# Optimization experiments

Hardware: AMD Instinct MI355X
Metric: run time of the kernel (lower is better)

Reference implementation:

```python
import jax, jax.numpy as jnp
import numpy as np

B, L_IN, D_MODEL, CONV_D, KSIZE = 16, 512, 384, 1536, 3
MEL_MAX = 4096
LN_EPS = 1e-5


def _conv1d_same(h, w, b):
    # h: [B, C_in, L], w: [C_out, C_in, K] -> [B, C_out, L]
    y = jax.lax.conv_general_dilated(h, w, window_strides=(1,), padding='SAME',
                                     dimension_numbers=('NCH', 'OIH', 'NCH'))
    return y + b[None, :, None]


def _layernorm(x, g, b):
    m = jnp.mean(x, -1, keepdims=True)
    v = jnp.mean((x - m) ** 2, -1, keepdims=True)
    return (x - m) * jax.lax.rsqrt(v + LN_EPS) * g + b


def _ffn(x, wa, ba, wb, bb):
    # Conv1D_FFT: conv(d_model->conv_d) ReLU conv(conv_d->d_model) ReLU
    h = jnp.transpose(x, (0, 2, 1))
    h = jax.nn.relu(_conv1d_same(h, wa, ba))
    h = jax.nn.relu(_conv1d_same(h, wb, bb))
    return jnp.transpose(h, (0, 2, 1))


def _dur_pred(x, w1, b1, w2, b2, g1, be1, w3, b3, w4, b4, g2, be2, wl, bl):
    h = _ffn(x, w1, b1, w2, b2)
    h = _layernorm(h, g1, be1)  # dropout is identity at eval
    h = _ffn(h, w3, b3, w4, b4)
    h = _layernorm(h, g2, be2)
    return (h @ wl + bl)[..., 0]  # [B, L_in], squeeze(-1)


def _length_regulate(x, dur, mel_max_len):
    # Equivalent to alignment @ x where alignment[b,t,j]=1 iff cum[b,j-1] <= t < cum[b,j],
    # padded with zeros out to mel_max_len (original pads output to mel_max_len).
    cum = jnp.cumsum(dur, axis=-1)                        # [B, L_in]
    total = cum[:, -1]                                    # [B]
    t = jnp.arange(mel_max_len, dtype=cum.dtype)          # [T]
    idx = jax.vmap(lambda c: jnp.searchsorted(c, t, side='right'))(cum)  # [B, T]
    idx = jnp.minimum(idx, x.shape[1] - 1)
    out = jnp.take_along_axis(x, idx[:, :, None], axis=1)  # [B, T, D]
    mask = (t[None, :] < total[:, None])[..., None]
    return out * mask


def setup_inputs() -> dict:
    key = jax.random.key(0)
    ks = jax.random.split(key, 8)
    def nrm(k, shape):
        return jax.random.normal(k, shape, jnp.float32) * 0.02
    return {
        'x': jax.random.normal(ks[0], (B, L_IN, D_MODEL), jnp.float32),
        'target': jax.random.randint(ks[1], (B, L_IN), 0, 8, jnp.int32),
        'mel_max_len': MEL_MAX,
        'w1': nrm(ks[2], (CONV_D, D_MODEL, KSIZE)), 'b1': jnp.zeros((CONV_D,), jnp.float32),
        'w2': nrm(ks[3], (D_MODEL, CONV_D, KSIZE)), 'b2': jnp.zeros((D_MODEL,), jnp.float32),
        'g1': jnp.ones((D_MODEL,), jnp.float32), 'be1': jnp.zeros((D_MODEL,), jnp.float32),
        'w3': nrm(ks[4], (CONV_D, D_MODEL, KSIZE)), 'b3': jnp.zeros((CONV_D,), jnp.float32),
        'w4': nrm(ks[5], (D_MODEL, CONV_D, KSIZE)), 'b4': jnp.zeros((D_MODEL,), jnp.float32),
        'g2': jnp.ones((D_MODEL,), jnp.float32), 'be2': jnp.zeros((D_MODEL,), jnp.float32),
        'wl': nrm(ks[6], (D_MODEL, 1)), 'bl': jnp.zeros((1,), jnp.float32),
    }


def reference(x, target, mel_max_len, w1, b1, w2, b2, g1, be1, w3, b3, w4, b4, g2, be2, wl, bl):
    dur_preds = _dur_pred(x, w1, b1, w2, b2, g1, be1, w3, b3, w4, b4, g2, be2, wl, bl)
    output = _length_regulate(x, target, mel_max_len)
    return (output, dur_preds)
```

## Files before the change

### kernel.cpp

```cpp
#include <hip/hip_runtime.h>
#include <hip/hip_bf16.h>
#include <cstddef>
#include <cstdint>

#define NB 16
#define LIN 512
#define DM 384
#define DC 1536
#define MELMAX 4096
#define LN_EPS 1e-5f

typedef __bf16 bf16x8 __attribute__((ext_vector_type(8)));
typedef float f32x4 __attribute__((ext_vector_type(4)));

#define GL2LDS(gp, lp)                                                                \
    __builtin_amdgcn_global_load_lds((const __attribute__((address_space(1))) void*)(gp), \
                                     (__attribute__((address_space(3))) void*)(lp), 16, 0, 0)

__device__ __forceinline__ float wred(float v) {
#pragma unroll
    for (int m = 32; m >= 1; m >>= 1) v += __shfl_xor(v, m, 64);
    return v;
}

__device__ __forceinline__ unsigned short f2bf(float f) {
    __hip_bfloat16 h = __float2bfloat16(f);
    return *reinterpret_cast<unsigned short*>(&h);
}

__device__ __forceinline__ float bf2f(unsigned short u) {
    return __uint_as_float(((unsigned)u) << 16);
}


__global__ void cumsum_kernel(const int* __restrict__ tgt, int* __restrict__ cum) {
    __shared__ int s[LIN];
    const int b = blockIdx.x, tid = threadIdx.x;
    s[tid] = tgt[b * LIN + tid];
    __syncthreads();
    for (int off = 1; off < LIN; off <<= 1) {
        int v = (tid >= off) ? s[tid - off] : 0;
        __syncthreads();
        s[tid] += v;
        __syncthreads();
    }
    cum[b * LIN + tid] = s[tid];
}


__global__ __launch_bounds__(256) void gather_kernel(const float* __restrict__ x,
                                                     const int* __restrict__ cum,
                                                     float* __restrict__ out) {
    const int wid = (blockIdx.x * 256 + threadIdx.x) >> 6;
    const int lane = threadIdx.x & 63;
    const int b = wid >> 12;
    const int t = wid & (MELMAX - 1);
    const int* c = cum + b * LIN;
    const int total = c[LIN - 1];
    float4* orow = reinterpret_cast<float4*>(out + ((size_t)b * MELMAX + t) * DM);
    if (t < total) {
        int lo = 0, hi = LIN;
        while (lo < hi) { int mid = (lo + hi) >> 1; if (c[mid] > t) hi = mid; else lo = mid + 1; }
        const int idx = lo < (LIN - 1) ? lo : (LIN - 1);
        const float4* xrow = reinterpret_cast<const float4*>(x + ((size_t)b * LIN + idx) * DM);
#pragma unroll
        for (int j = 0; j < 2; ++j) {
            const int p = lane + 64 * j;
            if (p < DM / 4) orow[p] = xrow[p];
        }
    } else {
        const float4 z = make_float4(0.f, 0.f, 0.f, 0.f);
#pragma unroll
        for (int j = 0; j < 2; ++j) {
            const int p = lane + 64 * j;
            if (p < DM / 4) orow[p] = z;
        }
    }
}


#define ZPAD_BLKS 96
#define CASTX_BLKS 3072
#define WCAST_BLKS 2304

__global__ void prep_kernel(const float* __restrict__ x, unsigned short* __restrict__ xb,
                            unsigned short* __restrict__ hbig, unsigned short* __restrict__ h2b,
                            const float* __restrict__ w1, const float* __restrict__ w2,
                            const float* __restrict__ w3, const float* __restrict__ w4,
                            unsigned short* __restrict__ o1, unsigned short* __restrict__ o2,
                            unsigned short* __restrict__ o3, unsigned short* __restrict__ o4) {
    const int bid = blockIdx.x, tid = threadIdx.x;
    if (bid < ZPAD_BLKS) {
        const int buf = bid >> 5, rem = bid & 31;
        const int b = rem >> 1, row = (rem & 1) ? (LIN + 1) : 0;
        unsigned short* p = buf == 0 ? xb : (buf == 1 ? hbig : h2b);
        const int rl = buf == 1 ? DC : DM;
        unsigned short* base = p + ((size_t)b * (LIN + 2) + row) * rl;
        for (int c = tid; c < rl; c += 256) base[c] = 0;
        return;
    }
    if (bid < ZPAD_BLKS + CASTX_BLKS) {
        const int idx = (bid - ZPAD_BLKS) * 256 + tid;
        const float4 v = reinterpret_cast<const float4*>(x)[idx];
        const int e = idx * 4;
        const int b = e / (LIN * DM);
        const int rem = e - b * (LIN * DM);
        const int l = rem / DM;
        const int c = rem - l * DM;
        ushort4 o;
        o.x = f2bf(v.x); o.y = f2bf(v.y); o.z = f2bf(v.z); o.w = f2bf(v.w);
        *reinterpret_cast<ushort4*>(xb + ((size_t)b * (LIN + 2) + l + 1) * DM + c) = o;
        return;
    }
    const int j = bid - ZPAD_BLKS - CASTX_BLKS;
    const int which = j / WCAST_BLKS;
    const int idx = (j - which * WCAST_BLKS) * 256 + tid;
    const float* w = which == 0 ? w1 : which == 1 ? w2 : which == 2 ? w3 : w4;
    unsigned short* gg = which == 0 ? o1 : which == 1 ? o2 : which == 2 ? o3 : o4;
    const int CI = (which == 0 || which == 2) ? DM : DC;
    const int co = idx / CI, ci = idx - co * CI;
    const float* p = w + (size_t)idx * 3;
    unsigned short* o = gg + (size_t)co * (3 * CI) + ci;
    o[0 * CI] = f2bf(p[0]);
    o[1 * CI] = f2bf(p[1]);
    o[2 * CI] = f2bf(p[2]);
}


template <int CI, int CO, int BN>
__global__ __launch_bounds__(256, 2) void conv_mfma_kernel(const unsigned short* __restrict__ in,
                                                           const unsigned short* __restrict__ wg,
                                                           const float* __restrict__ bias,
                                                           unsigned short* __restrict__ out) {
    constexpr int BM = 128, BK = 32;
    constexpr int KC = CI / BK;
    constexpr int AGRP = 12;
    constexpr int GPT = BN / 16;
    constexpr int BGRP = 3 * GPT;
    constexpr int NW_N = BN / 32;
    constexpr int NT = CO / BN;
    constexpr int NCONV = NB * (LIN / BM) * NT;

    __shared__ __align__(16) unsigned short As[2][AGRP * 512];
    __shared__ __align__(16) unsigned short Bs[2][BGRP * 512];

    const int tid = threadIdx.x;
    const int lane = tid & 63;
    const int wv = tid >> 6;

    const int orig = blockIdx.x;
    const int q = NCONV >> 3, xcd = orig & 7, o = orig >> 3;
    const int wgid = xcd * q + o;

    const int mg = wgid / NT;
    const int nt = wgid - mg * NT;
    const int b = mg >> 2;
    const int l0 = (mg & 3) * BM;
    const int n0 = nt * BN;

    const int wr = wv >> 1, wc = wv & 1;

    const unsigned short* inb = in + (size_t)b * (LIN + 2) * CI;

    f32x4 acc[4][NW_N];
#pragma unroll
    for (int m = 0; m < 4; ++m)
#pragma unroll
        for (int n = 0; n < NW_N; ++n) acc[m][n] = (f32x4){0.f, 0.f, 0.f, 0.f};

    const int lrow = lane >> 2;
    const int lch = lane & 3;
    const int fr = lane & 15, kg = lane >> 4;

    const unsigned short* aroot = inb + (size_t)l0 * CI + lch * 8;
    const unsigned short* broot = wg + (size_t)n0 * (3 * CI) + lch * 8;

#define STAGE(c, kb)                                                                      \
    do {                                                                                  \
        const unsigned short* abase = aroot + (kb) * BK;                                  \
        _Pragma("unroll")                                                                 \
        for (int g = wv; g < AGRP; g += 4) {                                              \
            const int sg = g < 9 ? g : 0;    \
            GL2LDS(abase + (size_t)(sg * 16 + lrow) * CI, &As[c][g * 512]);               \
        }                                                                                 \
        const unsigned short* bbase = broot + (kb) * BK;                                  \
        _Pragma("unroll")                                                                 \
        for (int g2 = wv; g2 < BGRP; g2 += 4) {                                           \
            const int t = g2 / GPT, gr = g2 - t * GPT;                                    \
            GL2LDS(bbase + (size_t)(gr * 16 + lrow) * (3 * CI) + (size_t)t * CI,          \
                   &Bs[c][g2 * 512]);                                                     \
        }                                                                                 \
    } while (0)

#define COMPUTE(c)                                                                        \
    do {                                                                                  \
        _Pragma("unroll")                                                                 \
        for (int t = 0; t < 3; ++t) {                                                     \
            bf16x8 aF[4], bF[NW_N];                                                       \
            _Pragma("unroll")                                                             \
            for (int m = 0; m < 4; ++m)                                                   \
                aF[m] = *reinterpret_cast<const bf16x8*>(                                 \
                    &As[c][(t + wr * 64 + m * 16 + fr) * BK + kg * 8]);                   \
            _Pragma("unroll")                                                             \
            for (int n = 0; n < NW_N; ++n)                                                \
                bF[n] = *reinterpret_cast<const bf16x8*>(                                 \
                    &Bs[c][(t * BN + wc * (BN / 2) + n * 16 + fr) * BK + kg * 8]);        \
            _Pragma("unroll")                                                             \
            for (int m = 0; m < 4; ++m)                                                   \
                _Pragma("unroll")                                                         \
                for (int n = 0; n < NW_N; ++n)                                            \
                    acc[m][n] =                                                           \
                        __builtin_amdgcn_mfma_f32_16x16x32_bf16(aF[m], bF[n], acc[m][n],  \
                                                                0, 0, 0);                 \
        }                                                                                 \
    } while (0)

    STAGE(0, 0);
    STAGE(1, 1);
#pragma unroll 1
    for (int kb = 0; kb < KC; ++kb) {
        const int cur = kb & 1;
        if constexpr (BN == 128)
            asm volatile("s_waitcnt vmcnt(9)" ::: "memory");
        else
            asm volatile("s_waitcnt vmcnt(6)" ::: "memory");
        __builtin_amdgcn_sched_barrier(0);
        __builtin_amdgcn_s_barrier();
        __builtin_amdgcn_sched_barrier(0);
        COMPUTE(cur);
        asm volatile("s_waitcnt lgkmcnt(0)" ::: "memory");
        __builtin_amdgcn_sched_barrier(0);
        __builtin_amdgcn_s_barrier();
        __builtin_amdgcn_sched_barrier(0);
        int nk = kb + 2;
        if (nk >= KC) nk -= KC;
        STAGE(cur, nk);
    }
#undef STAGE
#undef COMPUTE

    const int fq = lane >> 4;
    float bv[NW_N];
#pragma unroll
    for (int n = 0; n < NW_N; ++n) bv[n] = bias[n0 + wc * (BN / 2) + n * 16 + fr];
    unsigned short* outb = out + (size_t)b * (LIN + 2) * CO;
#pragma unroll
    for (int m = 0; m < 4; ++m)
#pragma unroll
        for (int qy = 0; qy < 4; ++qy) {
            const int grow = l0 + wr * 64 + m * 16 + fq * 4 + qy + 1;
            unsigned short* orow = outb + (size_t)grow * CO + n0 + wc * (BN / 2) + fr;
#pragma unroll
            for (int n = 0; n < NW_N; ++n) {
                const float v = fmaxf(acc[m][n][qy] + bv[n], 0.f);
                orow[n * 16] = f2bf(v);
            }
        }
}


__global__ void ln_kernel(unsigned short* __restrict__ h, const float* __restrict__ g,
                          const float* __restrict__ be) {
    const int row = blockIdx.x, lane = threadIdx.x;
    const int b = row >> 9, l = row & (LIN - 1);
    unsigned short* hr = h + ((size_t)b * (LIN + 2) + l + 1) * DM;
    float v[6];
    float s = 0.f;
#pragma unroll
    for (int j = 0; j < 6; ++j) { v[j] = bf2f(hr[lane + 64 * j]); s += v[j]; }
    s = wred(s);
    const float mean = s * (1.f / DM);
    float vs = 0.f;
#pragma unroll
    for (int j = 0; j < 6; ++j) { const float d = v[j] - mean; vs += d * d; }
    vs = wred(vs);
    const float rstd = rsqrtf(vs * (1.f / DM) + LN_EPS);
#pragma unroll
    for (int j = 0; j < 6; ++j) {
        const int c = lane + 64 * j;
        hr[c] = f2bf((v[j] - mean) * rstd * g[c] + be[c]);
    }
}


__global__ void ln_linear_kernel(const unsigned short* __restrict__ h, const float* __restrict__ g,
                                 const float* __restrict__ be, const float* __restrict__ wl,
                                 const float* __restrict__ bl, float* __restrict__ dur) {
    const int row = blockIdx.x, lane = threadIdx.x;
    const int b = row >> 9, l = row & (LIN - 1);
    const unsigned short* hr = h + ((size_t)b * (LIN + 2) + l + 1) * DM;
    float v[6];
    float s = 0.f;
#pragma unroll
    for (int j = 0; j < 6; ++j) { v[j] = bf2f(hr[lane + 64 * j]); s += v[j]; }
    s = wred(s);
    const float mean = s * (1.f / DM);
    float vs = 0.f;
#pragma unroll
    for (int j = 0; j < 6; ++j) { const float d = v[j] - mean; vs += d * d; }
    vs = wred(vs);
    const float rstd = rsqrtf(vs * (1.f / DM) + LN_EPS);
    float dot = 0.f;
#pragma unroll
    for (int j = 0; j < 6; ++j) {
        const int c = lane + 64 * j;
        dot += ((v[j] - mean) * rstd * g[c] + be[c]) * wl[c];
    }
    dot = wred(dot);
    if (lane == 0) dur[row] = dot + bl[0];
}


extern "C" void kernel_launch(void* const* d_in, const int* in_sizes, int n_in,
                              void* d_out, int out_size, void* d_ws, size_t ws_size,
                              hipStream_t stream) {
    const float* x   = (const float*)d_in[0];
    const int*   tgt = (const int*)d_in[1];
    const float* w1  = (const float*)d_in[3];
    const float* b1  = (const float*)d_in[4];
    const float* w2  = (const float*)d_in[5];
    const float* b2  = (const float*)d_in[6];
    const float* g1  = (const float*)d_in[7];
    const float* be1 = (const float*)d_in[8];
    const float* w3  = (const float*)d_in[9];
    const float* b3  = (const float*)d_in[10];
    const float* w4  = (const float*)d_in[11];
    const float* b4  = (const float*)d_in[12];
    const float* g2  = (const float*)d_in[13];
    const float* be2 = (const float*)d_in[14];
    const float* wl  = (const float*)d_in[15];
    const float* bl  = (const float*)d_in[16];

    float* out = (float*)d_out;
    float* dur = out + (size_t)NB * MELMAX * DM;

    unsigned short* ws = (unsigned short*)d_ws;
    unsigned short* xb   = ws;
    unsigned short* hbig = xb + (size_t)NB * (LIN + 2) * DM;
    unsigned short* h2b  = hbig + (size_t)NB * (LIN + 2) * DC;
    unsigned short* wg1  = h2b + (size_t)NB * (LIN + 2) * DM;
    unsigned short* wg2  = wg1 + (size_t)DC * 3 * DM;
    unsigned short* wg3  = wg2 + (size_t)DM * 3 * DC;
    unsigned short* wg4  = wg3 + (size_t)DC * 3 * DM;
    int* cum = (int*)(wg4 + (size_t)DM * 3 * DC);

    cumsum_kernel<<<NB, LIN, 0, stream>>>(tgt, cum);
    gather_kernel<<<(NB * MELMAX) / 4, 256, 0, stream>>>(x, cum, out);

    prep_kernel<<<ZPAD_BLKS + CASTX_BLKS + 4 * WCAST_BLKS, 256, 0, stream>>>(
        x, xb, hbig, h2b, w1, w2, w3, w4, wg1, wg2, wg3, wg4);

    conv_mfma_kernel<DM, DC, 128><<<NB * (LIN / 128) * (DC / 128), 256, 0, stream>>>(xb, wg1, b1, hbig);
    conv_mfma_kernel<DC, DM, 64><<<NB * (LIN / 128) * (DM / 64), 256, 0, stream>>>(hbig, wg2, b2, h2b);
    ln_kernel<<<NB * LIN, 64, 0, stream>>>(h2b, g1, be1);
    conv_mfma_kernel<DM, DC, 128><<<NB * (LIN / 128) * (DC / 128), 256, 0, stream>>>(h2b, wg3, b3, hbig);
    conv_mfma_kernel<DC, DM, 64><<<NB * (LIN / 128) * (DM / 64), 256, 0, stream>>>(hbig, wg4, b4, xb);
    ln_linear_kernel<<<NB * LIN, 64, 0, stream>>>(xb, g2, be2, wl, bl, dur);
}
```

Baseline: 223.9 us.

## Swizzle conv LDS tiles, fix BN at 64, raise occupancy and MFMA priority

Fixes the conv tile width at 64 for all four convolutions, which doubles the block count for the d_model to conv_d convs. It trims the A-tile halo groups from 12 to 9, which removes the dummy duplicate loads. It applies an XOR swizzle to A-tile LDS columns and stores B tiles in a fragment-major layout to reduce LDS bank conflicts on the fragment reads. It also raises launch bounds to 3 blocks per CU, wraps MFMAs in s_setprio, and adjusts vmcnt waits per wave to match the new per-wave load counts. The narrower tile costs more A-tile reloads for the wide convs.

```diff
diff --git a/kernel.cpp b/kernel.cpp
--- a/kernel.cpp
+++ b/kernel.cpp
@@ -127,14 +127,14 @@
 }
 
 
-template <int CI, int CO, int BN>
-__global__ __launch_bounds__(256, 2) void conv_mfma_kernel(const unsigned short* __restrict__ in,
+template <int CI, int CO>
+__global__ __launch_bounds__(256, 3) void conv_mfma_kernel(const unsigned short* __restrict__ in,
                                                            const unsigned short* __restrict__ wg,
                                                            const float* __restrict__ bias,
                                                            unsigned short* __restrict__ out) {
-    constexpr int BM = 128, BK = 32;
+    constexpr int BM = 128, BN = 64, BK = 32;
     constexpr int KC = CI / BK;
-    constexpr int AGRP = 12;
+    constexpr int AGRP = 9;
     constexpr int GPT = BN / 16;
     constexpr int BGRP = 3 * GPT;
     constexpr int NW_N = BN / 32;
@@ -172,22 +172,23 @@
     const int lch = lane & 3;
     const int fr = lane & 15, kg = lane >> 4;
 
-    const unsigned short* aroot = inb + (size_t)l0 * CI + lch * 8;
-    const unsigned short* broot = wg + (size_t)n0 * (3 * CI) + lch * 8;
+    const unsigned short* aroot = inb + (size_t)l0 * CI;
+    const unsigned short* broot = wg + (size_t)n0 * (3 * CI);
+
+    const int aswz = (lch ^ (lrow & 3)) * 8;
+    const int bfr = lane & 15, bkg = lane >> 4;
 
 #define STAGE(c, kb)                                                                      \
     do {                                                                                  \
         const unsigned short* abase = aroot + (kb) * BK;                                  \
         _Pragma("unroll")                                                                 \
-        for (int g = wv; g < AGRP; g += 4) {                                              \
-            const int sg = g < 9 ? g : 0;    \
-            GL2LDS(abase + (size_t)(sg * 16 + lrow) * CI, &As[c][g * 512]);               \
-        }                                                                                 \
+        for (int g = wv; g < AGRP; g += 4)                                                \
+            GL2LDS(abase + (size_t)(g * 16 + lrow) * CI + aswz, &As[c][g * 512]);         \
         const unsigned short* bbase = broot + (kb) * BK;                                  \
         _Pragma("unroll")                                                                 \
         for (int g2 = wv; g2 < BGRP; g2 += 4) {                                           \
             const int t = g2 / GPT, gr = g2 - t * GPT;                                    \
-            GL2LDS(bbase + (size_t)(gr * 16 + lrow) * (3 * CI) + (size_t)t * CI,          \
+            GL2LDS(bbase + (size_t)(gr * 16 + bfr) * (3 * CI) + (size_t)t * CI + bkg * 8, \
                    &Bs[c][g2 * 512]);                                                     \
         }                                                                                 \
     } while (0)
@@ -198,13 +199,16 @@
         for (int t = 0; t < 3; ++t) {                                                     \
             bf16x8 aF[4], bF[NW_N];                                                       \
             _Pragma("unroll")                                                             \
-            for (int m = 0; m < 4; ++m)                                                   \
+            for (int m = 0; m < 4; ++m) {                                                 \
+                const int r = t + wr * 64 + m * 16 + fr;                                  \
                 aF[m] = *reinterpret_cast<const bf16x8*>(                                 \
-                    &As[c][(t + wr * 64 + m * 16 + fr) * BK + kg * 8]);                   \
+                    &As[c][r * BK + ((kg ^ (r & 3)) * 8)]);                               \
+            }                                                                             \
             _Pragma("unroll")                                                             \
             for (int n = 0; n < NW_N; ++n)                                                \
                 bF[n] = *reinterpret_cast<const bf16x8*>(                                 \
-                    &Bs[c][(t * BN + wc * (BN / 2) + n * 16 + fr) * BK + kg * 8]);        \
+                    &Bs[c][(t * GPT + wc * NW_N + n) * 512 + kg * 128 + fr * 8]);         \
+            __builtin_amdgcn_s_setprio(1);                                                \
             _Pragma("unroll")                                                             \
             for (int m = 0; m < 4; ++m)                                                   \
                 _Pragma("unroll")                                                         \
@@ -212,6 +216,7 @@
                     acc[m][n] =                                                           \
                         __builtin_amdgcn_mfma_f32_16x16x32_bf16(aF[m], bF[n], acc[m][n],  \
                                                                 0, 0, 0);                 \
+            __builtin_amdgcn_s_setprio(0);                                                \
         }                                                                                 \
     } while (0)
 
@@ -220,10 +225,10 @@
 #pragma unroll 1
     for (int kb = 0; kb < KC; ++kb) {
         const int cur = kb & 1;
-        if constexpr (BN == 128)
-            asm volatile("s_waitcnt vmcnt(9)" ::: "memory");
+        if (wv == 0)
+            asm volatile("s_waitcnt vmcnt(6)" ::: "memory");
         else
-            asm volatile("s_waitcnt vmcnt(6)" ::: "memory");
+            asm volatile("s_waitcnt vmcnt(5)" ::: "memory");
         __builtin_amdgcn_sched_barrier(0);
         __builtin_amdgcn_s_barrier();
         __builtin_amdgcn_sched_barrier(0);
@@ -350,10 +355,10 @@
     prep_kernel<<<ZPAD_BLKS + CASTX_BLKS + 4 * WCAST_BLKS, 256, 0, stream>>>(
         x, xb, hbig, h2b, w1, w2, w3, w4, wg1, wg2, wg3, wg4);
 
-    conv_mfma_kernel<DM, DC, 128><<<NB * (LIN / 128) * (DC / 128), 256, 0, stream>>>(xb, wg1, b1, hbig);
-    conv_mfma_kernel<DC, DM, 64><<<NB * (LIN / 128) * (DM / 64), 256, 0, stream>>>(hbig, wg2, b2, h2b);
+    conv_mfma_kernel<DM, DC><<<NB * (LIN / 128) * (DC / 64), 256, 0, stream>>>(xb, wg1, b1, hbig);
+    conv_mfma_kernel<DC, DM><<<NB * (LIN / 128) * (DM / 64), 256, 0, stream>>>(hbig, wg2, b2, h2b);
     ln_kernel<<<NB * LIN, 64, 0, stream>>>(h2b, g1, be1);
-    conv_mfma_kernel<DM, DC, 128><<<NB * (LIN / 128) * (DC / 128), 256, 0, stream>>>(h2b, wg3, b3, hbig);
-    conv_mfma_kernel<DC, DM, 64><<<NB * (LIN / 128) * (DM / 64), 256, 0, stream>>>(hbig, wg4, b4, xb);
+    conv_mfma_kernel<DM, DC><<<NB * (LIN / 128) * (DC / 64), 256, 0, stream>>>(h2b, wg3, b3, hbig);
+    conv_mfma_kernel<DC, DM><<<NB * (LIN / 128) * (DM / 64), 256, 0, stream>>>(hbig, wg4, b4, xb);
     ln_linear_kernel<<<NB * LIN, 64, 0, stream>>>(xb, g2, be2, wl, bl, dur);
 }
```

Result: slower. 235.5 us (+5.2%).

## Load conv weight fragments directly into registers and vectorize weight cast

Applied to the files above, without the earlier changes.

Weight (B operand) tiles no longer go through LDS: each wave loads its bf16 MFMA fragments straight from global memory into double-buffered registers, and the k-loop is unrolled by two so the register buffers alternate. The weight-cast prep kernel now handles 8 input channels per thread with float4 loads and uint4 stores instead of scalar accesses. This is meant to cut LDS traffic and LDS reads for B and to speed up the prep pass. In exchange it raises register pressure and issues uncoalesced global fragment loads, and the vmcnt waits were retuned to match.

```diff
diff --git a/kernel.cpp b/kernel.cpp
--- a/kernel.cpp
+++ b/kernel.cpp
@@ -81,7 +81,7 @@
 
 #define ZPAD_BLKS 96
 #define CASTX_BLKS 3072
-#define WCAST_BLKS 2304
+#define WCAST_BLKS 288
 
 __global__ void prep_kernel(const float* __restrict__ x, unsigned short* __restrict__ xb,
                             unsigned short* __restrict__ hbig, unsigned short* __restrict__ h2b,
@@ -118,12 +118,19 @@
     const float* w = which == 0 ? w1 : which == 1 ? w2 : which == 2 ? w3 : w4;
     unsigned short* gg = which == 0 ? o1 : which == 1 ? o2 : which == 2 ? o3 : o4;
     const int CI = (which == 0 || which == 2) ? DM : DC;
-    const int co = idx / CI, ci = idx - co * CI;
-    const float* p = w + (size_t)idx * 3;
-    unsigned short* o = gg + (size_t)co * (3 * CI) + ci;
-    o[0 * CI] = f2bf(p[0]);
-    o[1 * CI] = f2bf(p[1]);
-    o[2 * CI] = f2bf(p[2]);
+    const int OCT = CI / 8;
+    const int co = idx / OCT, ci0 = (idx - co * OCT) * 8;
+    const float4* p4 = reinterpret_cast<const float4*>(w + (size_t)(co * CI + ci0) * 3);
+    float v[24];
+#pragma unroll
+    for (int q = 0; q < 6; ++q) *reinterpret_cast<float4*>(&v[q * 4]) = p4[q];
+    unsigned short tmp[3][8];
+#pragma unroll
+    for (int e = 0; e < 24; ++e) tmp[e % 3][e / 3] = f2bf(v[e]);
+    unsigned short* ob = gg + (size_t)co * (3 * CI) + ci0;
+#pragma unroll
+    for (int t = 0; t < 3; ++t)
+        *reinterpret_cast<uint4*>(ob + (size_t)t * CI) = *reinterpret_cast<const uint4*>(tmp[t]);
 }
 
 
@@ -134,15 +141,14 @@
                                                            unsigned short* __restrict__ out) {
     constexpr int BM = 128, BK = 32;
     constexpr int KC = CI / BK;
+    constexpr int AGRP_REAL = 9;
     constexpr int AGRP = 12;
-    constexpr int GPT = BN / 16;
-    constexpr int BGRP = 3 * GPT;
     constexpr int NW_N = BN / 32;
+    constexpr int NBF = 3 * NW_N;
     constexpr int NT = CO / BN;
     constexpr int NCONV = NB * (LIN / BM) * NT;
 
     __shared__ __align__(16) unsigned short As[2][AGRP * 512];
-    __shared__ __align__(16) unsigned short Bs[2][BGRP * 512];
 
     const int tid = threadIdx.x;
     const int lane = tid & 63;
@@ -173,71 +179,97 @@
     const int fr = lane & 15, kg = lane >> 4;
 
     const unsigned short* aroot = inb + (size_t)l0 * CI + lch * 8;
-    const unsigned short* broot = wg + (size_t)n0 * (3 * CI) + lch * 8;
+    const unsigned short* bfrag = wg + (size_t)(n0 + wc * (BN / 2) + fr) * (3 * CI) + kg * 8;
+
+    bf16x8 bfA[NBF], bfB[NBF];
 
 #define STAGE(c, kb)                                                                      \
     do {                                                                                  \
         const unsigned short* abase = aroot + (kb) * BK;                                  \
         _Pragma("unroll")                                                                 \
         for (int g = wv; g < AGRP; g += 4) {                                              \
-            const int sg = g < 9 ? g : 0;    \
+            const int sg = g < AGRP_REAL ? g : 0; \
             GL2LDS(abase + (size_t)(sg * 16 + lrow) * CI, &As[c][g * 512]);               \
         }                                                                                 \
-        const unsigned short* bbase = broot + (kb) * BK;                                  \
+    } while (0)
+
+#define BLOAD(DST, kb)                                                                    \
+    do {                                                                                  \
         _Pragma("unroll")                                                                 \
-        for (int g2 = wv; g2 < BGRP; g2 += 4) {                                           \
-            const int t = g2 / GPT, gr = g2 - t * GPT;                                    \
-            GL2LDS(bbase + (size_t)(gr * 16 + lrow) * (3 * CI) + (size_t)t * CI,          \
-                   &Bs[c][g2 * 512]);                                                     \
-        }                                                                                 \
+        for (int t = 0; t < 3; ++t)                                                       \
+            _Pragma("unroll")                                                             \
+            for (int n = 0; n < NW_N; ++n)                                                \
+                DST[t * NW_N + n] = *reinterpret_cast<const bf16x8*>(                     \
+                    bfrag + (size_t)(n * 16) * (3 * CI) + t * CI + (kb) * BK);            \
     } while (0)
 
-#define COMPUTE(c)                                                                        \
+#define COMPUTE(c, BF)                                                                    \
     do {                                                                                  \
         _Pragma("unroll")                                                                 \
         for (int t = 0; t < 3; ++t) {                                                     \
-            bf16x8 aF[4], bF[NW_N];                                                       \
+            bf16x8 aF[4];                                                                 \
             _Pragma("unroll")                                                             \
             for (int m = 0; m < 4; ++m)                                                   \
                 aF[m] = *reinterpret_cast<const bf16x8*>(                                 \
                     &As[c][(t + wr * 64 + m * 16 + fr) * BK + kg * 8]);                   \
             _Pragma("unroll")                                                             \
-            for (int n = 0; n < NW_N; ++n)                                                \
-                bF[n] = *reinterpret_cast<const bf16x8*>(                                 \
-                    &Bs[c][(t * BN + wc * (BN / 2) + n * 16 + fr) * BK + kg * 8]);        \
-            _Pragma("unroll")                                                             \
             for (int m = 0; m < 4; ++m)                                                   \
                 _Pragma("unroll")                                                         \
                 for (int n = 0; n < NW_N; ++n)                                            \
-                    acc[m][n] =                                                           \
-                        __builtin_amdgcn_mfma_f32_16x16x32_bf16(aF[m], bF[n], acc[m][n],  \
-                                                                0, 0, 0);                 \
+                    acc[m][n] = __builtin_amdgcn_mfma_f32_16x16x32_bf16(                  \
+                        aF[m], BF[t * NW_N + n], acc[m][n], 0, 0, 0);                     \
         }                                                                                 \
     } while (0)
 
+#define WAITV                                                                             \
+    do {                                                                                  \
+        if constexpr (BN == 128)                                                          \
+            asm volatile("s_waitcnt vmcnt(15)" ::: "memory");                             \
+        else                                                                              \
+            asm volatile("s_waitcnt vmcnt(9)" ::: "memory");                              \
+    } while (0)
+
+    BLOAD(bfA, 0);
     STAGE(0, 0);
+    BLOAD(bfB, 1);
     STAGE(1, 1);
 #pragma unroll 1
-    for (int kb = 0; kb < KC; ++kb) {
-        const int cur = kb & 1;
-        if constexpr (BN == 128)
-            asm volatile("s_waitcnt vmcnt(9)" ::: "memory");
-        else
-            asm volatile("s_waitcnt vmcnt(6)" ::: "memory");
+    for (int kb = 0; kb < KC; kb += 2) {
+        WAITV;
         __builtin_amdgcn_sched_barrier(0);
         __builtin_amdgcn_s_barrier();
         __builtin_amdgcn_sched_barrier(0);
-        COMPUTE(cur);
+        COMPUTE(0, bfA);
         asm volatile("s_waitcnt lgkmcnt(0)" ::: "memory");
         __builtin_amdgcn_sched_barrier(0);
         __builtin_amdgcn_s_barrier();
         __builtin_amdgcn_sched_barrier(0);
-        int nk = kb + 2;
-        if (nk >= KC) nk -= KC;
-        STAGE(cur, nk);
+        {
+            int nk = kb + 2;
+            if (nk >= KC) nk -= KC;
+            BLOAD(bfA, nk);
+            STAGE(0, nk);
+        }
+        WAITV;
+        __builtin_amdgcn_sched_barrier(0);
+        __builtin_amdgcn_s_barrier();
+        __builtin_amdgcn_sched_barrier(0);
+        COMPUTE(1, bfB);
+        asm volatile("s_waitcnt lgkmcnt(0)" ::: "memory");
+        __builtin_amdgcn_sched_barrier(0);
+        __builtin_amdgcn_s_barrier();
+        __builtin_amdgcn_sched_barrier(0);
+        {
+            int nk = kb + 3;
+            if (nk >= KC) nk -= KC;
+            BLOAD(bfB, nk);
+            STAGE(1, nk);
+        }
     }
 #undef STAGE
+#undef BLOAD
 #undef COMPUTE
+#undef WAITV
 
     const int fq = lane >> 4;
     float bv[NW_N];
```

Measured after the change: 353.7 us. 58.0% more time.
